# Kernel tuning notes

Measured on AMD Instinct MI355X. Metric: run time of the kernel, lower is better.

## Reference

```python
import jax, jax.numpy as jnp
import numpy as np

C = 1.0  # Poincare ball curvature


def _artanh(x):
    return jnp.arctanh(jnp.clip(x, -1 + 1e-5, 1 - 1e-5))


def _expmap0(u, c=C):
    sc = jnp.sqrt(jnp.float32(c))
    n = jnp.clip(jnp.linalg.norm(u, axis=-1, keepdims=True), 1e-15)
    return jnp.tanh(sc * n) * u / (sc * n)


def _logmap0(x, c=C):
    sc = jnp.sqrt(jnp.float32(c))
    n = jnp.clip(jnp.linalg.norm(x, axis=-1, keepdims=True), 1e-15)
    return _artanh(sc * n) * x / (sc * n)


def _mobius_add(x, y, c=C):
    x2 = jnp.sum(x * x, -1, keepdims=True)
    y2 = jnp.sum(y * y, -1, keepdims=True)
    xy = jnp.sum(x * y, -1, keepdims=True)
    num = (1 + 2 * c * xy + c * y2) * x + (1 - c * x2) * y
    den = 1 + 2 * c * xy + c * c * x2 * y2
    return num / jnp.clip(den, 1e-15)


def _mobius_matvec(M, x, c=C):
    sc = jnp.sqrt(jnp.float32(c))
    xn = jnp.clip(jnp.linalg.norm(x, axis=-1, keepdims=True), 1e-15)
    Mx = x @ M.T
    Mxn = jnp.clip(jnp.linalg.norm(Mx, axis=-1, keepdims=True), 1e-15)
    return jnp.tanh(Mxn / xn * _artanh(sc * xn)) * Mx / (sc * Mxn)


def _dist2_all(x, y, c=C):
    # x: [N, D] points on ball, y: [K, D] codebook points -> [N, K] squared dists
    # dist(x,y) = 2/sqrt(c) * artanh(sqrt(c) * ||(-x) (+) y||)
    # ||(-x) (+) y|| computed from dot products only (no [N,K,D] intermediate):
    #   (-x) (+) y = (a*(-x) + b*y) / den,
    #   a = 1 - 2c<x,y> + c|y|^2,  b = 1 - c|x|^2,  den = 1 - 2c<x,y> + c^2|x|^2|y|^2
    x2 = jnp.sum(x * x, -1)[:, None]           # [N,1]
    y2 = jnp.sum(y * y, -1)[None, :]           # [1,K]
    xy = x @ y.T                               # [N,K] (the big matmul)
    a = 1 - 2 * c * xy + c * y2
    b = 1 - c * x2
    den = 1 - 2 * c * xy + c * c * x2 * y2
    num2 = a * a * x2 - 2 * a * b * xy + b * b * y2
    norm = jnp.sqrt(jnp.clip(num2, 0.0)) / jnp.clip(den, 1e-15)
    d = (2.0 / jnp.sqrt(jnp.float32(c))) * _artanh(jnp.sqrt(jnp.float32(c)) * norm)
    return d * d


def setup_inputs() -> dict:
    key = jax.random.key(0)
    k0, k1, k2, k3, k4 = jax.random.split(key, 5)
    B, S, D, K = 16, 128, 128, 32000
    v_tangent = 0.1 * jax.random.normal(k0, (B, S, D), jnp.float32)
    code_points = _expmap0(0.1 * jax.random.normal(k1, (K, D), jnp.float32))
    W = jax.random.normal(k2, (D, D), jnp.float32) / jnp.sqrt(jnp.float32(D))
    b = 0.01 * jax.random.normal(k3, (D,), jnp.float32)
    freq = jax.random.uniform(k4, (K,), jnp.float32) * 1000.0
    fb = jnp.log(freq + 1.0)
    freq_bias = (fb - fb.mean()) * 0.5
    return {"v_tangent": v_tangent, "code_points": code_points, "W": W,
            "b": b, "freq_bias": freq_bias, "temperature": jnp.float32(1.0)}


def reference(v_tangent, code_points, W, b, freq_bias, temperature):
    batch_shape = v_tangent.shape[:-1]
    D = v_tangent.shape[-1]
    v = v_tangent.reshape(-1, D)
    # tiny hyperbolic linear layer (1-layer Poincare MLP = Mobius matvec + Mobius bias add)
    p = _expmap0(v)
    p = _mobius_add(_mobius_matvec(W, p), _expmap0(b[None, :]))
    v = _logmap0(p)
    # back onto the manifold, distance-based logits vs full codebook
    p = _expmap0(v)
    logits = -_dist2_all(p, code_points) / (temperature * temperature)
    logits = logits + freq_bias[None, :]
    return logits.reshape(*batch_shape, -1)
```

## Files before the change

kernel.cpp:

```cpp
#include <hip/hip_runtime.h>
#include <hip/hip_bf16.h>


typedef __attribute__((ext_vector_type(8))) short short8;
typedef __attribute__((ext_vector_type(4))) float f32x4;
typedef unsigned short u16;

__device__ inline float bits2f(unsigned u){ union{unsigned u; float f;} x; x.u=u; return x.f; }
__device__ inline u16 f2bf(float f){
  union { float f; unsigned u; } x; x.f = f;
  unsigned r = x.u + 0x7fff + ((x.u >> 16) & 1);
  return (u16)(r >> 16);
}
__device__ inline void bfsplit(float f, u16 &h, u16 &l){
  u16 hb = f2bf(f);
  float hf = bits2f(((unsigned)hb) << 16);
  h = hb;
  l = f2bf(f - hf);
}

__device__ inline float wred(float x){
#pragma unroll
  for (int off = 32; off; off >>= 1) x += __shfl_xor(x, off, 64);
  return x;
}

__device__ inline float dotW(const float* __restrict__ w, const float* __restrict__ p){
  float m = 0.f;
#pragma unroll
  for (int i = 0; i < 32; ++i){
    float4 u = *(const float4*)(w + 4*i);
    const float* q = p + 4*i;
    m = fmaf(u.x, q[0], m); m = fmaf(u.y, q[1], m);
    m = fmaf(u.z, q[2], m); m = fmaf(u.w, q[3], m);
  }
  return m;
}

__global__ __launch_bounds__(64) void prep_kernel(
    const float* __restrict__ vt, const float* __restrict__ Wm,
    const float* __restrict__ bias,
    u16* __restrict__ ahi, u16* __restrict__ alo, float* __restrict__ x2o)
{
  const int row = blockIdx.x, lane = threadIdx.x;
  const int e0 = 2*lane;
  const float CLIP = 0.99999f;

  float v0 = vt[row*128 + e0];
  float v1 = vt[row*128 + e0 + 1];
  float n1 = fmaxf(sqrtf(wred(v0*v0 + v1*v1)), 1e-15f);
  float s1 = tanhf(n1)/n1;
  float p0 = s1*v0, p1 = s1*v1;
  __shared__ float sP[128];
  sP[e0] = p0; sP[e0+1] = p1;
  __syncthreads();
  float xn = fmaxf(sqrtf(wred(p0*p0 + p1*p1)), 1e-15f);
  float mx0 = dotW(Wm + e0*128, sP);
  float mx1 = dotW(Wm + (e0+1)*128, sP);
  float Mxn = fmaxf(sqrtf(wred(mx0*mx0 + mx1*mx1)), 1e-15f);
  float smv = tanhf((Mxn/xn) * atanhf(fminf(xn, CLIP))) / Mxn;
  float m0 = smv*mx0, m1 = smv*mx1;
  float b0 = bias[e0], b1 = bias[e0+1];
  float nb = fmaxf(sqrtf(wred(b0*b0 + b1*b1)), 1e-15f);
  float sb = tanhf(nb)/nb;
  float eb0 = sb*b0, eb1 = sb*b1;
  float x2m = wred(m0*m0 + m1*m1);
  float y2e = wred(eb0*eb0 + eb1*eb1);
  float xy  = wred(m0*eb0 + m1*eb1);
  float ca = 1.f + 2.f*xy + y2e;
  float cb = 1.f - x2m;
  float den = fmaxf(1.f + 2.f*xy + x2m*y2e, 1e-15f);
  float q0 = (ca*m0 + cb*eb0)/den, q1 = (ca*m1 + cb*eb1)/den;
  float n2 = fmaxf(sqrtf(wred(q0*q0 + q1*q1)), 1e-15f);
  float u = atanhf(fminf(n2, CLIP));
  float sv = u/n2;
  float w0v = sv*q0, w1v = sv*q1;
  float n3 = fmaxf(sqrtf(wred(w0v*w0v + w1v*w1v)), 1e-15f);
  float s3 = tanhf(n3)/n3;
  float P0 = s3*w0v, P1 = s3*w1v;
  float x2v = wred(P0*P0 + P1*P1);
  u16 h0, l0, h1, l1;
  bfsplit(P0, h0, l0); bfsplit(P1, h1, l1);
  ahi[row*128 + e0] = h0; ahi[row*128 + e0 + 1] = h1;
  alo[row*128 + e0] = l0; alo[row*128 + e0 + 1] = l1;
  if (lane == 0) x2o[row] = x2v;
}

__global__ __launch_bounds__(256) void y2_kernel(
    const float* __restrict__ code, float* __restrict__ y2o)
{
  int k = blockIdx.x*256 + threadIdx.x;
  const float* r = code + (size_t)k*128;
  float s = 0.f;
#pragma unroll
  for (int i = 0; i < 32; ++i){
    float4 u = *(const float4*)(r + 4*i);
    s = fmaf(u.x,u.x,s); s = fmaf(u.y,u.y,s);
    s = fmaf(u.z,u.z,s); s = fmaf(u.w,u.w,s);
  }
  y2o[k] = s;
}

#define SBS 136

__global__ __launch_bounds__(256, 4) void decode_main(
    const float* __restrict__ code, const u16* __restrict__ ahi_g,
    const u16* __restrict__ alo_g, const float* __restrict__ x2g,
    const float* __restrict__ y2g, const float* __restrict__ fbg,
    const float* __restrict__ tempg, float* __restrict__ outp)
{
  __shared__ u16 sBh[64*SBS];
  __shared__ u16 sBl[64*SBS];
  const int tid  = threadIdx.x;
  const int wave = tid >> 6, lane = tid & 63;
  const int quad = lane >> 4, l16 = lane & 15;
  const int m0 = blockIdx.y*64 + wave*16;
  const int arow = m0 + l16;

  short8 ah[4], al[4];
#pragma unroll
  for (int ks = 0; ks < 4; ++ks){
    ah[ks] = *(const short8*)(ahi_g + arow*128 + ks*32 + quad*8);
    al[ks] = *(const short8*)(alo_g + arow*128 + ks*32 + quad*8);
  }
  float x2v[4], ntb[4], b2[4];
#pragma unroll
  for (int r = 0; r < 4; ++r){
    float xv = x2g[m0 + quad*4 + r];
    x2v[r] = xv;
    float bb = 1.f - xv;
    ntb[r] = -2.f*bb;
    b2[r]  = bb*bb;
  }
  const float tmp  = tempg[0];
  const float nit2 = -1.f/(tmp*tmp);
  const int n_base = blockIdx.x*256;

  for (int rnd = 0; rnd < 4; ++rnd){
    const int n0r = n_base + rnd*64;
    __syncthreads();
#pragma unroll
    for (int i = 0; i < 8; ++i){
      int id = tid + i*256;
      int c = id >> 5, sg = id & 31;
      float4 u = *(const float4*)(code + (size_t)(n0r + c)*128 + sg*4);
      u16 h0,h1,h2,h3,l0,l1,l2,l3;
      bfsplit(u.x,h0,l0); bfsplit(u.y,h1,l1);
      bfsplit(u.z,h2,l2); bfsplit(u.w,h3,l3);
      ushort4 hv; hv.x=h0; hv.y=h1; hv.z=h2; hv.w=h3;
      ushort4 lv; lv.x=l0; lv.y=l1; lv.z=l2; lv.w=l3;
      *(ushort4*)(&sBh[c*SBS + sg*4]) = hv;
      *(ushort4*)(&sBl[c*SBS + sg*4]) = lv;
    }
    __syncthreads();
#pragma unroll
    for (int ct = 0; ct < 4; ++ct){
      const int ccol = ct*16 + l16;
      short8 bh[4], bl[4];
#pragma unroll
      for (int ks = 0; ks < 4; ++ks){
        bh[ks] = *(const short8*)(&sBh[ccol*SBS + ks*32 + quad*8]);
        bl[ks] = *(const short8*)(&sBl[ccol*SBS + ks*32 + quad*8]);
      }
      f32x4 acch = {0.f,0.f,0.f,0.f}, accx = {0.f,0.f,0.f,0.f};
#pragma unroll
      for (int ks = 0; ks < 4; ++ks){
        acch = __builtin_amdgcn_mfma_f32_16x16x32_bf16(ah[ks], bh[ks], acch, 0, 0, 0);
        accx = __builtin_amdgcn_mfma_f32_16x16x32_bf16(ah[ks], bl[ks], accx, 0, 0, 0);
        accx = __builtin_amdgcn_mfma_f32_16x16x32_bf16(al[ks], bh[ks], accx, 0, 0, 0);
      }
      const int col = n_base + rnd*64 + ct*16 + l16;
      const float y2v  = y2g[col];
      const float fbv  = fbg[col];
      const float y2p1 = 1.f + y2v;
#pragma unroll
      for (int r = 0; r < 4; ++r){
        float t   = acch[r] + accx[r];
        float two = t + t;
        float a   = y2p1 - two;
        float den = fmaf(x2v[r], y2v, 1.f - two);
        float dc  = fmaxf(den, 1e-15f);
        float num2 = fmaf(a*x2v[r], a, fmaf(ntb[r]*t, a, b2[r]*y2v));
        float sq  = sqrtf(fmaxf(num2, 0.f));
        float s   = fminf(sq, 0.99999f*dc);
        float d   = __logf(__fdividef(dc + s, dc - s));
        float outv = fmaf(d*d, nit2, fbv);
        outp[(size_t)(m0 + quad*4 + r)*32000 + col] = outv;
      }
    }
  }
}

extern "C" void kernel_launch(void* const* d_in, const int* in_sizes, int n_in,
                              void* d_out, int out_size, void* d_ws, size_t ws_size,
                              hipStream_t stream) {
  const float* vt   = (const float*)d_in[0];
  const float* code = (const float*)d_in[1];
  const float* Wm   = (const float*)d_in[2];
  const float* bias = (const float*)d_in[3];
  const float* fb   = (const float*)d_in[4];
  const float* temp = (const float*)d_in[5];
  float* outp = (float*)d_out;

  char* ws = (char*)d_ws;
  u16*   ahi = (u16*)ws;
  u16*   alo = (u16*)(ws + 512*1024);
  float* x2  = (float*)(ws + 1024*1024);
  float* y2  = (float*)(ws + 1024*1024 + 8192);

  prep_kernel<<<2048, 64, 0, stream>>>(vt, Wm, bias, ahi, alo, x2);
  y2_kernel<<<125, 256, 0, stream>>>(code, y2);
  dim3 grid(125, 32);
  decode_main<<<grid, 256, 0, stream>>>(code, ahi, alo, x2, y2, fb, temp, outp);
}
```

Before: 448.6 us.

## Pre-split codebook to bf16 hi/lo once, swap MFMA operands for float4 stores

Codebook bf16 hi/lo splitting moves out of the main kernel into a separate pass that also computes y2, so each decode block loads pre-split bf16 data instead of recomputing the split for all 32 row tiles. MFMA operand order is swapped so each lane owns four consecutive output columns, which allows vectorized float4 output stores and float4 y2/bias loads. The grid is transposed so blocks sharing a codebook tile run adjacently, and the occupancy hint drops from 4 to 3 blocks. This adds 16 MB of workspace traffic for the split codebook.

```diff
diff --git a/kernel.cpp b/kernel.cpp
--- a/kernel.cpp
+++ b/kernel.cpp
@@ -22,6 +22,11 @@
 __device__ inline float wred(float x){
 #pragma unroll
   for (int off = 32; off; off >>= 1) x += __shfl_xor(x, off, 64);
+  return x;
+}
+__device__ inline float wred32(float x){
+#pragma unroll
+  for (int off = 16; off; off >>= 1) x += __shfl_xor(x, off, 64);
   return x;
 }
 
@@ -86,35 +91,40 @@
   if (lane == 0) x2o[row] = x2v;
 }
 
-__global__ __launch_bounds__(256) void y2_kernel(
-    const float* __restrict__ code, float* __restrict__ y2o)
+__global__ __launch_bounds__(256) void split_y2_kernel(
+    const float* __restrict__ code, u16* __restrict__ Bh,
+    u16* __restrict__ Bl, float* __restrict__ y2o)
 {
-  int k = blockIdx.x*256 + threadIdx.x;
-  const float* r = code + (size_t)k*128;
-  float s = 0.f;
-#pragma unroll
-  for (int i = 0; i < 32; ++i){
-    float4 u = *(const float4*)(r + 4*i);
-    s = fmaf(u.x,u.x,s); s = fmaf(u.y,u.y,s);
-    s = fmaf(u.z,u.z,s); s = fmaf(u.w,u.w,s);
-  }
-  y2o[k] = s;
+  const int c = threadIdx.x & 31, r = threadIdx.x >> 5;
+  const int row = blockIdx.x*8 + r;
+  float4 u = *(const float4*)(code + (size_t)row*128 + c*4);
+  u16 h0,h1,h2,h3,l0,l1,l2,l3;
+  bfsplit(u.x,h0,l0); bfsplit(u.y,h1,l1);
+  bfsplit(u.z,h2,l2); bfsplit(u.w,h3,l3);
+  ushort4 hv; hv.x=h0; hv.y=h1; hv.z=h2; hv.w=h3;
+  ushort4 lv; lv.x=l0; lv.y=l1; lv.z=l2; lv.w=l3;
+  *(ushort4*)(Bh + (size_t)row*128 + c*4) = hv;
+  *(ushort4*)(Bl + (size_t)row*128 + c*4) = lv;
+  float s = fmaf(u.x,u.x, fmaf(u.y,u.y, fmaf(u.z,u.z, u.w*u.w)));
+  s = wred32(s);
+  if (c == 0) y2o[row] = s;
 }
 
 #define SBS 136
 
-__global__ __launch_bounds__(256, 4) void decode_main(
-    const float* __restrict__ code, const u16* __restrict__ ahi_g,
-    const u16* __restrict__ alo_g, const float* __restrict__ x2g,
-    const float* __restrict__ y2g, const float* __restrict__ fbg,
-    const float* __restrict__ tempg, float* __restrict__ outp)
+__global__ __launch_bounds__(256, 3) void decode_main(
+    const u16* __restrict__ Bh_g, const u16* __restrict__ Bl_g,
+    const u16* __restrict__ ahi_g, const u16* __restrict__ alo_g,
+    const float* __restrict__ x2g, const float* __restrict__ y2g,
+    const float* __restrict__ fbg, const float* __restrict__ tempg,
+    float* __restrict__ outp)
 {
   __shared__ u16 sBh[64*SBS];
   __shared__ u16 sBl[64*SBS];
   const int tid  = threadIdx.x;
   const int wave = tid >> 6, lane = tid & 63;
   const int quad = lane >> 4, l16 = lane & 15;
-  const int m0 = blockIdx.y*64 + wave*16;
+  const int m0 = blockIdx.x*64 + wave*16;
   const int arow = m0 + l16;
 
   short8 ah[4], al[4];
@@ -123,34 +133,24 @@
     ah[ks] = *(const short8*)(ahi_g + arow*128 + ks*32 + quad*8);
     al[ks] = *(const short8*)(alo_g + arow*128 + ks*32 + quad*8);
   }
-  float x2v[4], ntb[4], b2[4];
-#pragma unroll
-  for (int r = 0; r < 4; ++r){
-    float xv = x2g[m0 + quad*4 + r];
-    x2v[r] = xv;
-    float bb = 1.f - xv;
-    ntb[r] = -2.f*bb;
-    b2[r]  = bb*bb;
-  }
+  const float xv  = x2g[arow];
+  const float bb  = 1.f - xv;
+  const float ntb = -2.f*bb;
+  const float b2  = bb*bb;
   const float tmp  = tempg[0];
   const float nit2 = -1.f/(tmp*tmp);
-  const int n_base = blockIdx.x*256;
+  const int n_base = blockIdx.y*256;
 
   for (int rnd = 0; rnd < 4; ++rnd){
     const int n0r = n_base + rnd*64;
     __syncthreads();
 #pragma unroll
-    for (int i = 0; i < 8; ++i){
+    for (int i = 0; i < 4; ++i){
       int id = tid + i*256;
-      int c = id >> 5, sg = id & 31;
-      float4 u = *(const float4*)(code + (size_t)(n0r + c)*128 + sg*4);
-      u16 h0,h1,h2,h3,l0,l1,l2,l3;
-      bfsplit(u.x,h0,l0); bfsplit(u.y,h1,l1);
-      bfsplit(u.z,h2,l2); bfsplit(u.w,h3,l3);
-      ushort4 hv; hv.x=h0; hv.y=h1; hv.z=h2; hv.w=h3;
-      ushort4 lv; lv.x=l0; lv.y=l1; lv.z=l2; lv.w=l3;
-      *(ushort4*)(&sBh[c*SBS + sg*4]) = hv;
-      *(ushort4*)(&sBl[c*SBS + sg*4]) = lv;
+      int c = id >> 4, sg = id & 15;
+      size_t goff = (size_t)(n0r + c)*128 + sg*8;
+      *(uint4*)(&sBh[c*SBS + sg*8]) = *(const uint4*)(Bh_g + goff);
+      *(uint4*)(&sBl[c*SBS + sg*8]) = *(const uint4*)(Bl_g + goff);
     }
     __syncthreads();
 #pragma unroll
@@ -165,28 +165,29 @@
       f32x4 acch = {0.f,0.f,0.f,0.f}, accx = {0.f,0.f,0.f,0.f};
 #pragma unroll
       for (int ks = 0; ks < 4; ++ks){
-        acch = __builtin_amdgcn_mfma_f32_16x16x32_bf16(ah[ks], bh[ks], acch, 0, 0, 0);
-        accx = __builtin_amdgcn_mfma_f32_16x16x32_bf16(ah[ks], bl[ks], accx, 0, 0, 0);
-        accx = __builtin_amdgcn_mfma_f32_16x16x32_bf16(al[ks], bh[ks], accx, 0, 0, 0);
+        acch = __builtin_amdgcn_mfma_f32_16x16x32_bf16(bh[ks], ah[ks], acch, 0, 0, 0);
+        accx = __builtin_amdgcn_mfma_f32_16x16x32_bf16(bl[ks], ah[ks], accx, 0, 0, 0);
+        accx = __builtin_amdgcn_mfma_f32_16x16x32_bf16(bh[ks], al[ks], accx, 0, 0, 0);
       }
-      const int col = n_base + rnd*64 + ct*16 + l16;
-      const float y2v  = y2g[col];
-      const float fbv  = fbg[col];
-      const float y2p1 = 1.f + y2v;
+      const int cbase = n0r + ct*16 + quad*4;
+      const float4 y2v4 = *(const float4*)(y2g + cbase);
+      const float4 fbv4 = *(const float4*)(fbg + cbase);
+      float4 o;
 #pragma unroll
       for (int r = 0; r < 4; ++r){
+        float y2v = ((const float*)&y2v4)[r];
         float t   = acch[r] + accx[r];
         float two = t + t;
-        float a   = y2p1 - two;
-        float den = fmaf(x2v[r], y2v, 1.f - two);
+        float a   = (1.f + y2v) - two;
+        float den = fmaf(xv, y2v, 1.f - two);
         float dc  = fmaxf(den, 1e-15f);
-        float num2 = fmaf(a*x2v[r], a, fmaf(ntb[r]*t, a, b2[r]*y2v));
+        float num2 = fmaf(a*xv, a, fmaf(ntb*t, a, b2*y2v));
         float sq  = sqrtf(fmaxf(num2, 0.f));
         float s   = fminf(sq, 0.99999f*dc);
         float d   = __logf(__fdividef(dc + s, dc - s));
-        float outv = fmaf(d*d, nit2, fbv);
-        outp[(size_t)(m0 + quad*4 + r)*32000 + col] = outv;
+        ((float*)&o)[r] = fmaf(d*d, nit2, ((const float*)&fbv4)[r]);
       }
+      *(float4*)(outp + (size_t)arow*32000 + cbase) = o;
     }
   }
 }
@@ -207,9 +208,11 @@
   u16*   alo = (u16*)(ws + 512*1024);
   float* x2  = (float*)(ws + 1024*1024);
   float* y2  = (float*)(ws + 1024*1024 + 8192);
+  u16*   Bh  = (u16*)(ws + 1280*1024);
+  u16*   Bl  = (u16*)(ws + 1280*1024 + 8192*1024);
 
   prep_kernel<<<2048, 64, 0, stream>>>(vt, Wm, bias, ahi, alo, x2);
-  y2_kernel<<<125, 256, 0, stream>>>(code, y2);
-  dim3 grid(125, 32);
-  decode_main<<<grid, 256, 0, stream>>>(code, ahi, alo, x2, y2, fb, temp, outp);
-}
+  split_y2_kernel<<<4000, 256, 0, stream>>>(code, Bh, Bl, y2);
+  dim3 grid(32, 125);
+  decode_main<<<grid, 256, 0, stream>>>(Bh, Bl, ahi, alo, x2, y2, fb, temp, outp);
+}
```

Measured after the change: 446.4 us. About the same (-0.5%).
